# Kernel optimization log

Measured on AMD Instinct MI355X. Metric: run time of the kernel, lower is better.

## Reference

```python
import jax, jax.numpy as jnp
import numpy as np


def _gcn_conv(h, src, dst, W, b, n):
    # PyG GCNConv: XW, symmetric deg normalization (with self-loops already in src/dst), scatter-add, + bias
    hw = h @ W                                            # [n, out]
    deg = jax.ops.segment_sum(jnp.ones_like(src, dtype=h.dtype), dst, num_segments=n)
    dinv = jax.lax.rsqrt(deg)                             # deg >= 1 due to self loops
    coef = (dinv[src] * dinv[dst])[:, None]               # [E+n, 1]
    out = jax.ops.segment_sum(hw[src] * coef, dst, num_segments=n)
    return out + b


def setup_inputs() -> dict:
    key = jax.random.key(0)
    ks = jax.random.split(key, 8)
    num_users, num_items = 8192, 8192
    N = num_users + num_items
    E = 524288
    d, h1, h2, h3 = 128, 256, 128, 64
    x = jnp.arange(N, dtype=jnp.int64) if jax.config.jax_enable_x64 else jnp.arange(N, dtype=jnp.int32)
    edge_index = jax.random.randint(ks[0], (2, E), 0, N)
    emb = jax.random.normal(ks[1], (num_items + 1, d), dtype=jnp.float32)
    W1 = jax.random.normal(ks[2], (d, h1), dtype=jnp.float32) * 0.5
    b1 = jax.random.normal(ks[3], (h1,), dtype=jnp.float32) * 0.1
    W2 = jax.random.normal(ks[4], (h1, h2), dtype=jnp.float32) * 0.6
    b2 = jax.random.normal(ks[5], (h2,), dtype=jnp.float32) * 0.1
    Wl = jax.random.normal(ks[6], (h2, h3), dtype=jnp.float32) * 0.06
    bl = jax.random.normal(ks[7], (h3,), dtype=jnp.float32) * 0.1
    return {"x": x, "edge_index": edge_index, "num_users": num_users,
            "emb": emb, "W1": W1, "b1": b1, "W2": W2, "b2": b2, "Wl": Wl, "bl": bl}


def reference(x, edge_index, num_users, emb, W1, b1, W2, b2, Wl, bl):
    n = x.shape[0]
    # embedding lookup: users all use id 0, items use shifted ids
    users_e = jnp.broadcast_to(emb[0], (num_users, emb.shape[1]))
    items_e = emb[x[num_users:] - num_users + 1]
    h = jnp.concatenate([users_e, items_e], axis=0)       # [n, d]
    loops = jnp.arange(n, dtype=edge_index.dtype)
    src = jnp.concatenate([edge_index[0], loops])
    dst = jnp.concatenate([edge_index[1], loops])
    h = jax.nn.relu(_gcn_conv(h, src, dst, W1, b1, n))    # dropout p=0 -> identity
    h = jax.nn.relu(_gcn_conv(h, src, dst, W2, b2, n))
    h = jax.nn.relu(h @ Wl + bl)                          # linear + middle_function='relu'
    users = h[:num_users]
    items = h[num_users:]
    result = users @ items.T                              # [num_users, num_items]
    return jnp.clip(result, 1.0, 5.0)                     # end_function='clamp'
```

## Files before the change

### kernel.cpp

```cpp
#include <hip/hip_runtime.h>
#include <hip/hip_bf16.h>

#define CAP 96

typedef __attribute__((ext_vector_type(8))) short bf16x8;
typedef __attribute__((ext_vector_type(4))) float f32x4;

static __device__ __forceinline__ float bflo(unsigned int w) {
    union { unsigned int i; float f; } u; u.i = w << 16; return u.f;
}
static __device__ __forceinline__ float bfhi(unsigned int w) {
    union { unsigned int i; float f; } u; u.i = w & 0xffff0000u; return u.f;
}
static __device__ __forceinline__ unsigned short f2bf(float f) {
    __hip_bfloat16 h = __float2bfloat16(f);
    union { __hip_bfloat16 b; unsigned short s; } u; u.b = h; return u.s;
}

__global__ void scatter_kernel(const int* __restrict__ src, const int* __restrict__ dst,
                               int* __restrict__ wp, int* __restrict__ edges, int E) {
    int e = blockIdx.x * blockDim.x + threadIdx.x;
    if (e < E) {
        int d = dst[e];
        int p = atomicAdd(&wp[d], 1);
        if (p < CAP) edges[d * CAP + p] = src[e];
    }
}

__global__ void dinv_kernel(const int* __restrict__ wp, float* __restrict__ dinv, int n) {
    int v = blockIdx.x * blockDim.x + threadIdx.x;
    if (v < n) dinv[v] = rsqrtf((float)(wp[v] + 1));
}

__global__ void prep_kernel(const int* __restrict__ x, const float* __restrict__ emb,
                            const float* __restrict__ W1, const float* __restrict__ W2,
                            const float* __restrict__ Wl,
                            unsigned short* __restrict__ h0,
                            unsigned short* __restrict__ W1t,
                            unsigned short* __restrict__ W2t,
                            unsigned short* __restrict__ Wlt,
                            int* __restrict__ wp, int nu, int n) {
    int i = blockIdx.x * blockDim.x + threadIdx.x;
    int H = n * 16;
    if (i < H) {
        int node = i >> 4, c8 = i & 15;
        int row = (node < nu) ? 0 : (x[node] - nu + 1);
        float4 f0 = reinterpret_cast<const float4*>(emb)[(size_t)row * 32 + c8 * 2];
        float4 f1 = reinterpret_cast<const float4*>(emb)[(size_t)row * 32 + c8 * 2 + 1];
        union { unsigned short s[8]; uint4 v; } o;
        o.s[0] = f2bf(f0.x); o.s[1] = f2bf(f0.y); o.s[2] = f2bf(f0.z); o.s[3] = f2bf(f0.w);
        o.s[4] = f2bf(f1.x); o.s[5] = f2bf(f1.y); o.s[6] = f2bf(f1.z); o.s[7] = f2bf(f1.w);
        *reinterpret_cast<uint4*>(h0 + (size_t)node * 128 + c8 * 8) = o.v;
        return;
    }
    int j = i - H;
    if (j < 32768) {
        int nn = j >> 7, kk = j & 127;
        W1t[j] = f2bf(W1[kk * 256 + nn]);
        return;
    }
    if (j < 65536) {
        int jj = j - 32768;
        int nn = jj >> 8, kk = jj & 255;
        W2t[jj] = f2bf(W2[kk * 128 + nn]);
        return;
    }
    if (j < 73728) {
        int jj = j - 65536;
        int nn = jj >> 7, kk = jj & 127;
        Wlt[jj] = f2bf(Wl[kk * 64 + nn]);
        return;
    }
    int z = j - 73728;
    if (z < n) wp[z] = 0;
}

static __device__ __forceinline__ void agg_node_to_lds(
    const unsigned short* __restrict__ in, unsigned short* lds_row,
    int v, int lane, const int* __restrict__ cnt, const int* __restrict__ edges,
    const float* __restrict__ dinv, const float* __restrict__ bias, int relu) {
    int l16 = lane & 15;
    int g = lane >> 4;
    float acc[8] = {0.f, 0.f, 0.f, 0.f, 0.f, 0.f, 0.f, 0.f};
    int c = cnt[v];
    if (c > CAP) c = CAP;
    int s0 = v * CAP;
    int e = s0 + g;
    int end = s0 + c;
    for (; e + 12 < end; e += 16) {
        int sa = edges[e];
        int sb = edges[e + 4];
        int sc = edges[e + 8];
        int sd = edges[e + 12];
        float wa = dinv[sa], wb = dinv[sb], wc = dinv[sc], wd = dinv[sd];
        uint4 ra = *reinterpret_cast<const uint4*>(in + (size_t)sa * 128 + l16 * 8);
        uint4 rb = *reinterpret_cast<const uint4*>(in + (size_t)sb * 128 + l16 * 8);
        uint4 rc = *reinterpret_cast<const uint4*>(in + (size_t)sc * 128 + l16 * 8);
        uint4 rd = *reinterpret_cast<const uint4*>(in + (size_t)sd * 128 + l16 * 8);
        acc[0] = fmaf(wa, bflo(ra.x), acc[0]); acc[1] = fmaf(wa, bfhi(ra.x), acc[1]);
        acc[2] = fmaf(wa, bflo(ra.y), acc[2]); acc[3] = fmaf(wa, bfhi(ra.y), acc[3]);
        acc[4] = fmaf(wa, bflo(ra.z), acc[4]); acc[5] = fmaf(wa, bfhi(ra.z), acc[5]);
        acc[6] = fmaf(wa, bflo(ra.w), acc[6]); acc[7] = fmaf(wa, bfhi(ra.w), acc[7]);
        acc[0] = fmaf(wb, bflo(rb.x), acc[0]); acc[1] = fmaf(wb, bfhi(rb.x), acc[1]);
        acc[2] = fmaf(wb, bflo(rb.y), acc[2]); acc[3] = fmaf(wb, bfhi(rb.y), acc[3]);
        acc[4] = fmaf(wb, bflo(rb.z), acc[4]); acc[5] = fmaf(wb, bfhi(rb.z), acc[5]);
        acc[6] = fmaf(wb, bflo(rb.w), acc[6]); acc[7] = fmaf(wb, bfhi(rb.w), acc[7]);
        acc[0] = fmaf(wc, bflo(rc.x), acc[0]); acc[1] = fmaf(wc, bfhi(rc.x), acc[1]);
        acc[2] = fmaf(wc, bflo(rc.y), acc[2]); acc[3] = fmaf(wc, bfhi(rc.y), acc[3]);
        acc[4] = fmaf(wc, bflo(rc.z), acc[4]); acc[5] = fmaf(wc, bfhi(rc.z), acc[5]);
        acc[6] = fmaf(wc, bflo(rc.w), acc[6]); acc[7] = fmaf(wc, bfhi(rc.w), acc[7]);
        acc[0] = fmaf(wd, bflo(rd.x), acc[0]); acc[1] = fmaf(wd, bfhi(rd.x), acc[1]);
        acc[2] = fmaf(wd, bflo(rd.y), acc[2]); acc[3] = fmaf(wd, bfhi(rd.y), acc[3]);
        acc[4] = fmaf(wd, bflo(rd.z), acc[4]); acc[5] = fmaf(wd, bfhi(rd.z), acc[5]);
        acc[6] = fmaf(wd, bflo(rd.w), acc[6]); acc[7] = fmaf(wd, bfhi(rd.w), acc[7]);
    }
    for (; e < end; e += 4) {
        int sa = edges[e];
        float wa = dinv[sa];
        uint4 ra = *reinterpret_cast<const uint4*>(in + (size_t)sa * 128 + l16 * 8);
        acc[0] = fmaf(wa, bflo(ra.x), acc[0]); acc[1] = fmaf(wa, bfhi(ra.x), acc[1]);
        acc[2] = fmaf(wa, bflo(ra.y), acc[2]); acc[3] = fmaf(wa, bfhi(ra.y), acc[3]);
        acc[4] = fmaf(wa, bflo(ra.z), acc[4]); acc[5] = fmaf(wa, bfhi(ra.z), acc[5]);
        acc[6] = fmaf(wa, bflo(ra.w), acc[6]); acc[7] = fmaf(wa, bfhi(ra.w), acc[7]);
    }
#pragma unroll
    for (int d = 0; d < 8; ++d) {
        acc[d] += __shfl_xor(acc[d], 16, 64);
        acc[d] += __shfl_xor(acc[d], 32, 64);
    }
    if (g == 0) {
        float dv = dinv[v];
        uint4 sp = *reinterpret_cast<const uint4*>(in + (size_t)v * 128 + l16 * 8);
        float self[8] = {bflo(sp.x), bfhi(sp.x), bflo(sp.y), bfhi(sp.y),
                         bflo(sp.z), bfhi(sp.z), bflo(sp.w), bfhi(sp.w)};
        union { unsigned short s[8]; uint4 u; } o;
#pragma unroll
        for (int d = 0; d < 8; ++d) {
            float val = (acc[d] + dv * self[d]) * dv;
            if (bias) val += bias[l16 * 8 + d];
            if (relu) val = fmaxf(val, 0.f);
            o.s[d] = f2bf(val);
        }
        *reinterpret_cast<uint4*>(lds_row + l16 * 8) = o.u;
    }
}

__global__ __launch_bounds__(256) void fused_conv1_kernel(
    const unsigned short* __restrict__ h0b, unsigned short* __restrict__ hw2b,
    const int* __restrict__ cnt, const int* __restrict__ edges,
    const float* __restrict__ dinv,
    const unsigned short* __restrict__ W1t, const float* __restrict__ b1,
    const unsigned short* __restrict__ W2t) {
    __shared__ unsigned short zt[16][136];
    __shared__ unsigned short h1t[16][264];
    int wid = threadIdx.x >> 6, lane = threadIdx.x & 63;
    int base = blockIdx.x * 16;
#pragma unroll
    for (int q = 0; q < 4; ++q) {
        int loc = wid * 4 + q;
        agg_node_to_lds(h0b, &zt[loc][0], base + loc, lane, cnt, edges, dinv,
                        nullptr, 0);
    }
    __syncthreads();
    int lr = lane & 15, kg = (lane >> 4) * 8;
    int rq = (lane >> 4) * 4;
    {
        int bn = wid * 64;
        f32x4 acc[4] = {{0,0,0,0},{0,0,0,0},{0,0,0,0},{0,0,0,0}};
        for (int k0 = 0; k0 < 128; k0 += 32) {
            bf16x8 a = *reinterpret_cast<const bf16x8*>(&zt[lr][k0 + kg]);
#pragma unroll
            for (int c = 0; c < 4; ++c) {
                bf16x8 b = *reinterpret_cast<const bf16x8*>(W1t + (size_t)(bn + c * 16 + lr) * 128 + k0 + kg);
                acc[c] = __builtin_amdgcn_mfma_f32_16x16x32_bf16(a, b, acc[c], 0, 0, 0);
            }
        }
#pragma unroll
        for (int c = 0; c < 4; ++c) {
            int col = bn + c * 16 + lr;
            float bs = b1[col];
#pragma unroll
            for (int q = 0; q < 4; ++q) {
                float vv = fmaxf(acc[c][q] + bs, 0.f);
                h1t[rq + q][col] = f2bf(vv);
            }
        }
    }
    __syncthreads();
    {
        int bn = wid * 32;
        f32x4 acc[2] = {{0,0,0,0},{0,0,0,0}};
        for (int k0 = 0; k0 < 256; k0 += 32) {
            bf16x8 a = *reinterpret_cast<const bf16x8*>(&h1t[lr][k0 + kg]);
#pragma unroll
            for (int c = 0; c < 2; ++c) {
                bf16x8 b = *reinterpret_cast<const bf16x8*>(W2t + (size_t)(bn + c * 16 + lr) * 256 + k0 + kg);
                acc[c] = __builtin_amdgcn_mfma_f32_16x16x32_bf16(a, b, acc[c], 0, 0, 0);
            }
        }
#pragma unroll
        for (int c = 0; c < 2; ++c) {
            int col = bn + c * 16 + lr;
#pragma unroll
            for (int q = 0; q < 4; ++q)
                hw2b[(size_t)(base + rq + q) * 128 + col] = f2bf(acc[c][q]);
        }
    }
}

__global__ __launch_bounds__(256) void fused_conv2_kernel(
    const unsigned short* __restrict__ hw2b, unsigned short* __restrict__ h3b,
    const int* __restrict__ cnt, const int* __restrict__ edges,
    const float* __restrict__ dinv, const float* __restrict__ b2,
    const unsigned short* __restrict__ Wlt, const float* __restrict__ bl) {
    __shared__ unsigned short ht[16][136];
    int wid = threadIdx.x >> 6, lane = threadIdx.x & 63;
    int base = blockIdx.x * 16;
#pragma unroll
    for (int q = 0; q < 4; ++q) {
        int loc = wid * 4 + q;
        agg_node_to_lds(hw2b, &ht[loc][0], base + loc, lane, cnt, edges, dinv,
                        b2, 1);
    }
    __syncthreads();
    int lr = lane & 15, kg = (lane >> 4) * 8;
    int rq = (lane >> 4) * 4;
    f32x4 acc = {0, 0, 0, 0};
    for (int k0 = 0; k0 < 128; k0 += 32) {
        bf16x8 a = *reinterpret_cast<const bf16x8*>(&ht[lr][k0 + kg]);
        bf16x8 b = *reinterpret_cast<const bf16x8*>(Wlt + (size_t)(wid * 16 + lr) * 128 + k0 + kg);
        acc = __builtin_amdgcn_mfma_f32_16x16x32_bf16(a, b, acc, 0, 0, 0);
    }
    int col = wid * 16 + lr;
    float bs = bl[col];
#pragma unroll
    for (int q = 0; q < 4; ++q) {
        float vv = fmaxf(acc[q] + bs, 0.f);
        h3b[(size_t)(base + rq + q) * 64 + col] = f2bf(vv);
    }
}

__global__ __launch_bounds__(256) void final_gemm_kernel(
    const short* __restrict__ h3b, float* __restrict__ out, int nu, int ni) {
    __shared__ float tile[4][16][65];
    int wid = threadIdx.x >> 6, lane = threadIdx.x & 63;
    int row0 = blockIdx.x * 128 + (wid >> 1) * 64;
    int col0 = blockIdx.y * 128 + (wid & 1) * 64;
    int lr = lane & 15;
    int kg = (lane >> 4) * 8;
    const short* Au = h3b;
    const short* Bi = h3b + (size_t)nu * 64;
    bf16x8 a[4][2], b[4][2];
#pragma unroll
    for (int r = 0; r < 4; ++r)
#pragma unroll
        for (int kt = 0; kt < 2; ++kt) {
            a[r][kt] = *reinterpret_cast<const bf16x8*>(Au + (size_t)(row0 + r * 16 + lr) * 64 + kt * 32 + kg);
            b[r][kt] = *reinterpret_cast<const bf16x8*>(Bi + (size_t)(col0 + r * 16 + lr) * 64 + kt * 32 + kg);
        }
    f32x4 acc[4][4];
#pragma unroll
    for (int r = 0; r < 4; ++r)
#pragma unroll
        for (int c = 0; c < 4; ++c) {
            f32x4 z = {0.f, 0.f, 0.f, 0.f};
            z = __builtin_amdgcn_mfma_f32_16x16x32_bf16(a[r][0], b[c][0], z, 0, 0, 0);
            z = __builtin_amdgcn_mfma_f32_16x16x32_bf16(a[r][1], b[c][1], z, 0, 0, 0);
            acc[r][c] = z;
        }
    int rq = (lane >> 4) * 4;
    int orow = lane >> 4;
#pragma unroll
    for (int r = 0; r < 4; ++r) {
        __syncthreads();
#pragma unroll
        for (int c = 0; c < 4; ++c)
#pragma unroll
            for (int q = 0; q < 4; ++q) {
                float v = acc[r][c][q];
                v = fminf(fmaxf(v, 1.f), 5.f);
                tile[wid][rq + q][c * 16 + lr] = v;
            }
        __syncthreads();
#pragma unroll
        for (int rr = 0; rr < 4; ++rr) {
            float4 vv = *reinterpret_cast<const float4*>(&tile[wid][rr * 4 + orow][lr * 4]);
            *reinterpret_cast<float4*>(
                &out[(size_t)(row0 + r * 16 + rr * 4 + orow) * ni + col0 + lr * 4]) = vv;
        }
    }
}

extern "C" void kernel_launch(void* const* d_in, const int* in_sizes, int n_in,
                              void* d_out, int out_size, void* d_ws, size_t ws_size,
                              hipStream_t stream) {
    const int*   x   = (const int*)d_in[0];
    const int*   ei  = (const int*)d_in[1];
    const float* emb = (const float*)d_in[3];
    const float* W1  = (const float*)d_in[4];
    const float* b1  = (const float*)d_in[5];
    const float* W2  = (const float*)d_in[6];
    const float* b2  = (const float*)d_in[7];
    const float* Wl  = (const float*)d_in[8];
    const float* bl  = (const float*)d_in[9];
    float* out = (float*)d_out;

    const int n   = in_sizes[0];
    const int E   = in_sizes[1] / 2;
    const int h1d = in_sizes[5];
    const int d   = in_sizes[4] / h1d;
    const int embrows = in_sizes[3] / d;
    const int nu  = n - (embrows - 1);
    const int ni  = n - nu;

    const int* srcp = ei;
    const int* dstp = ei + E;

    char* w = (char*)d_ws;
    int*   wp      = (int*)(w + 0);
    float* dinv    = (float*)(w + (64 << 10));
    unsigned short* W1t = (unsigned short*)(w + (128 << 10));
    unsigned short* W2t = (unsigned short*)(w + (192 << 10));
    unsigned short* Wlt = (unsigned short*)(w + (256 << 10));
    int*   edges   = (int*)(w + (1 << 20));
    unsigned short* h0b  = (unsigned short*)(w + (8  << 20));
    unsigned short* hw2b = (unsigned short*)(w + (12 << 20));
    unsigned short* h3b  = (unsigned short*)(w + (16 << 20));

    {
        int total = n * 16 + 73728 + n;
        prep_kernel<<<(total + 255) / 256, 256, 0, stream>>>(
            x, emb, W1, W2, Wl, h0b, W1t, W2t, Wlt, wp, nu, n);
    }

    scatter_kernel<<<(E + 255) / 256, 256, 0, stream>>>(srcp, dstp, wp, edges, E);
    dinv_kernel<<<(n + 255) / 256, 256, 0, stream>>>(wp, dinv, n);

    fused_conv1_kernel<<<n / 16, 256, 0, stream>>>(
        h0b, hw2b, wp, edges, dinv, W1t, b1, W2t);

    fused_conv2_kernel<<<n / 16, 256, 0, stream>>>(
        hw2b, h3b, wp, edges, dinv, b2, Wlt, bl);

    {
        dim3 g(nu / 128, ni / 128);
        final_gemm_kernel<<<g, 256, 0, stream>>>((const short*)h3b, out, nu, ni);
    }
}
```

Baseline: 153.4 us.

## Split edge lists by user/item source to skip gathering identical user embeddings

Edges are bucketed per destination into separate user-source and item-source lists. In conv1 every user node shares the same embedding row, so the user-neighbour contribution collapses to a scalar sum of dinv times one row instead of a row gather per edge. This cuts roughly half the row gathers in the first aggregation and shrinks the embedding prep. The price is a second atomic counter array and per-type capacities of 64, which could truncate high-degree nodes differently than the old single cap of 96.

```diff
diff --git a/kernel.cpp b/kernel.cpp
--- a/kernel.cpp
+++ b/kernel.cpp
@@ -1,7 +1,8 @@
 #include <hip/hip_runtime.h>
 #include <hip/hip_bf16.h>
 
-#define CAP 96
+#define CAPU 64
+#define CAPI 64
 
 typedef __attribute__((ext_vector_type(8))) short bf16x8;
 typedef __attribute__((ext_vector_type(4))) float f32x4;
@@ -18,42 +19,65 @@
 }
 
 __global__ void scatter_kernel(const int* __restrict__ src, const int* __restrict__ dst,
-                               int* __restrict__ wp, int* __restrict__ edges, int E) {
+                               int* __restrict__ wpu, int* __restrict__ wpi,
+                               int* __restrict__ uedges, int* __restrict__ iedges,
+                               int nu, int E) {
     int e = blockIdx.x * blockDim.x + threadIdx.x;
     if (e < E) {
         int d = dst[e];
-        int p = atomicAdd(&wp[d], 1);
-        if (p < CAP) edges[d * CAP + p] = src[e];
-    }
-}
-
-__global__ void dinv_kernel(const int* __restrict__ wp, float* __restrict__ dinv, int n) {
+        int s = src[e];
+        if (s < nu) {
+            int p = atomicAdd(&wpu[d], 1);
+            if (p < CAPU) uedges[d * CAPU + p] = s;
+        } else {
+            int p = atomicAdd(&wpi[d], 1);
+            if (p < CAPI) iedges[d * CAPI + p] = s - nu;
+        }
+    }
+}
+
+__global__ void dinv_kernel(const int* __restrict__ wpu, const int* __restrict__ wpi,
+                            float* __restrict__ dinv, int n) {
     int v = blockIdx.x * blockDim.x + threadIdx.x;
-    if (v < n) dinv[v] = rsqrtf((float)(wp[v] + 1));
+    if (v < n) dinv[v] = rsqrtf((float)(wpu[v] + wpi[v] + 1));
 }
 
 __global__ void prep_kernel(const int* __restrict__ x, const float* __restrict__ emb,
                             const float* __restrict__ W1, const float* __restrict__ W2,
                             const float* __restrict__ Wl,
-                            unsigned short* __restrict__ h0,
+                            unsigned short* __restrict__ hi,
+                            unsigned short* __restrict__ h0u,
                             unsigned short* __restrict__ W1t,
                             unsigned short* __restrict__ W2t,
                             unsigned short* __restrict__ Wlt,
-                            int* __restrict__ wp, int nu, int n) {
+                            int* __restrict__ wpu, int* __restrict__ wpi,
+                            int nu, int n) {
     int i = blockIdx.x * blockDim.x + threadIdx.x;
-    int H = n * 16;
-    if (i < H) {
-        int node = i >> 4, c8 = i & 15;
-        int row = (node < nu) ? 0 : (x[node] - nu + 1);
+    int ni = n - nu;
+    int HI = ni * 16;
+    if (i < HI) {
+        int it = i >> 4, c8 = i & 15;
+        int row = x[nu + it] - nu + 1;
         float4 f0 = reinterpret_cast<const float4*>(emb)[(size_t)row * 32 + c8 * 2];
         float4 f1 = reinterpret_cast<const float4*>(emb)[(size_t)row * 32 + c8 * 2 + 1];
         union { unsigned short s[8]; uint4 v; } o;
         o.s[0] = f2bf(f0.x); o.s[1] = f2bf(f0.y); o.s[2] = f2bf(f0.z); o.s[3] = f2bf(f0.w);
         o.s[4] = f2bf(f1.x); o.s[5] = f2bf(f1.y); o.s[6] = f2bf(f1.z); o.s[7] = f2bf(f1.w);
-        *reinterpret_cast<uint4*>(h0 + (size_t)node * 128 + c8 * 8) = o.v;
+        *reinterpret_cast<uint4*>(hi + (size_t)it * 128 + c8 * 8) = o.v;
         return;
     }
-    int j = i - H;
+    int j = i - HI;
+    if (j < 16) {
+        int c8 = j;
+        float4 f0 = reinterpret_cast<const float4*>(emb)[c8 * 2];
+        float4 f1 = reinterpret_cast<const float4*>(emb)[c8 * 2 + 1];
+        union { unsigned short s[8]; uint4 v; } o;
+        o.s[0] = f2bf(f0.x); o.s[1] = f2bf(f0.y); o.s[2] = f2bf(f0.z); o.s[3] = f2bf(f0.w);
+        o.s[4] = f2bf(f1.x); o.s[5] = f2bf(f1.y); o.s[6] = f2bf(f1.z); o.s[7] = f2bf(f1.w);
+        *reinterpret_cast<uint4*>(h0u + c8 * 8) = o.v;
+        return;
+    }
+    j -= 16;
     if (j < 32768) {
         int nn = j >> 7, kk = j & 127;
         W1t[j] = f2bf(W1[kk * 256 + nn]);
@@ -72,31 +96,25 @@
         return;
     }
     int z = j - 73728;
-    if (z < n) wp[z] = 0;
-}
-
-static __device__ __forceinline__ void agg_node_to_lds(
-    const unsigned short* __restrict__ in, unsigned short* lds_row,
-    int v, int lane, const int* __restrict__ cnt, const int* __restrict__ edges,
-    const float* __restrict__ dinv, const float* __restrict__ bias, int relu) {
-    int l16 = lane & 15;
-    int g = lane >> 4;
-    float acc[8] = {0.f, 0.f, 0.f, 0.f, 0.f, 0.f, 0.f, 0.f};
-    int c = cnt[v];
-    if (c > CAP) c = CAP;
-    int s0 = v * CAP;
-    int e = s0 + g;
-    int end = s0 + c;
+    if (z < n) { wpu[z] = 0; return; }
+    z -= n;
+    if (z < n) { wpi[z] = 0; }
+}
+
+static __device__ __forceinline__ void gather_rows(
+    const unsigned short* __restrict__ in, int rofs,
+    const int* __restrict__ lst, int base, int cnt,
+    const float* __restrict__ dinv, int dofs,
+    int l16, int g, float acc[8]) {
+    int e = base + g, end = base + cnt;
     for (; e + 12 < end; e += 16) {
-        int sa = edges[e];
-        int sb = edges[e + 4];
-        int sc = edges[e + 8];
-        int sd = edges[e + 12];
-        float wa = dinv[sa], wb = dinv[sb], wc = dinv[sc], wd = dinv[sd];
-        uint4 ra = *reinterpret_cast<const uint4*>(in + (size_t)sa * 128 + l16 * 8);
-        uint4 rb = *reinterpret_cast<const uint4*>(in + (size_t)sb * 128 + l16 * 8);
-        uint4 rc = *reinterpret_cast<const uint4*>(in + (size_t)sc * 128 + l16 * 8);
-        uint4 rd = *reinterpret_cast<const uint4*>(in + (size_t)sd * 128 + l16 * 8);
+        int sa = lst[e], sb = lst[e + 4], sc = lst[e + 8], sd = lst[e + 12];
+        float wa = dinv[sa + dofs], wb = dinv[sb + dofs];
+        float wc = dinv[sc + dofs], wd = dinv[sd + dofs];
+        uint4 ra = *reinterpret_cast<const uint4*>(in + (size_t)(sa + rofs) * 128 + l16 * 8);
+        uint4 rb = *reinterpret_cast<const uint4*>(in + (size_t)(sb + rofs) * 128 + l16 * 8);
+        uint4 rc = *reinterpret_cast<const uint4*>(in + (size_t)(sc + rofs) * 128 + l16 * 8);
+        uint4 rd = *reinterpret_cast<const uint4*>(in + (size_t)(sd + rofs) * 128 + l16 * 8);
         acc[0] = fmaf(wa, bflo(ra.x), acc[0]); acc[1] = fmaf(wa, bfhi(ra.x), acc[1]);
         acc[2] = fmaf(wa, bflo(ra.y), acc[2]); acc[3] = fmaf(wa, bfhi(ra.y), acc[3]);
         acc[4] = fmaf(wa, bflo(ra.z), acc[4]); acc[5] = fmaf(wa, bfhi(ra.z), acc[5]);
@@ -115,51 +133,62 @@
         acc[6] = fmaf(wd, bflo(rd.w), acc[6]); acc[7] = fmaf(wd, bfhi(rd.w), acc[7]);
     }
     for (; e < end; e += 4) {
-        int sa = edges[e];
-        float wa = dinv[sa];
-        uint4 ra = *reinterpret_cast<const uint4*>(in + (size_t)sa * 128 + l16 * 8);
+        int sa = lst[e];
+        float wa = dinv[sa + dofs];
+        uint4 ra = *reinterpret_cast<const uint4*>(in + (size_t)(sa + rofs) * 128 + l16 * 8);
         acc[0] = fmaf(wa, bflo(ra.x), acc[0]); acc[1] = fmaf(wa, bfhi(ra.x), acc[1]);
         acc[2] = fmaf(wa, bflo(ra.y), acc[2]); acc[3] = fmaf(wa, bfhi(ra.y), acc[3]);
         acc[4] = fmaf(wa, bflo(ra.z), acc[4]); acc[5] = fmaf(wa, bfhi(ra.z), acc[5]);
         acc[6] = fmaf(wa, bflo(ra.w), acc[6]); acc[7] = fmaf(wa, bfhi(ra.w), acc[7]);
     }
-#pragma unroll
-    for (int d = 0; d < 8; ++d) {
-        acc[d] += __shfl_xor(acc[d], 16, 64);
-        acc[d] += __shfl_xor(acc[d], 32, 64);
-    }
-    if (g == 0) {
-        float dv = dinv[v];
-        uint4 sp = *reinterpret_cast<const uint4*>(in + (size_t)v * 128 + l16 * 8);
-        float self[8] = {bflo(sp.x), bfhi(sp.x), bflo(sp.y), bfhi(sp.y),
-                         bflo(sp.z), bfhi(sp.z), bflo(sp.w), bfhi(sp.w)};
-        union { unsigned short s[8]; uint4 u; } o;
-#pragma unroll
-        for (int d = 0; d < 8; ++d) {
-            float val = (acc[d] + dv * self[d]) * dv;
-            if (bias) val += bias[l16 * 8 + d];
-            if (relu) val = fmaxf(val, 0.f);
-            o.s[d] = f2bf(val);
-        }
-        *reinterpret_cast<uint4*>(lds_row + l16 * 8) = o.u;
-    }
 }
 
 __global__ __launch_bounds__(256) void fused_conv1_kernel(
-    const unsigned short* __restrict__ h0b, unsigned short* __restrict__ hw2b,
-    const int* __restrict__ cnt, const int* __restrict__ edges,
+    const unsigned short* __restrict__ hi, const unsigned short* __restrict__ h0u,
+    unsigned short* __restrict__ hw2b,
+    const int* __restrict__ wpu, const int* __restrict__ wpi,
+    const int* __restrict__ uedges, const int* __restrict__ iedges,
     const float* __restrict__ dinv,
     const unsigned short* __restrict__ W1t, const float* __restrict__ b1,
-    const unsigned short* __restrict__ W2t) {
+    const unsigned short* __restrict__ W2t, int nu) {
     __shared__ unsigned short zt[16][136];
     __shared__ unsigned short h1t[16][264];
     int wid = threadIdx.x >> 6, lane = threadIdx.x & 63;
+    int l16 = lane & 15, g = lane >> 4;
     int base = blockIdx.x * 16;
 #pragma unroll
     for (int q = 0; q < 4; ++q) {
-        int loc = wid * 4 + q;
-        agg_node_to_lds(h0b, &zt[loc][0], base + loc, lane, cnt, edges, dinv,
-                        nullptr, 0);
+        int v = base + wid * 4 + q;
+        float su = 0.f;
+        int cu = min(wpu[v], CAPU);
+        for (int u = lane; u < cu; u += 64) su += dinv[uedges[v * CAPU + u]];
+#pragma unroll
+        for (int off = 1; off < 64; off <<= 1) su += __shfl_xor(su, off, 64);
+        float acc[8] = {0.f, 0.f, 0.f, 0.f, 0.f, 0.f, 0.f, 0.f};
+        int ci = min(wpi[v], CAPI);
+        gather_rows(hi, 0, iedges, v * CAPI, ci, dinv, nu, l16, g, acc);
+#pragma unroll
+        for (int d = 0; d < 8; ++d) {
+            acc[d] += __shfl_xor(acc[d], 16, 64);
+            acc[d] += __shfl_xor(acc[d], 32, 64);
+        }
+        if (g == 0) {
+            float dv = dinv[v];
+            const unsigned short* selfp = (v < nu) ? h0u : (hi + (size_t)(v - nu) * 128);
+            uint4 sp = *reinterpret_cast<const uint4*>(selfp + l16 * 8);
+            uint4 hu = *reinterpret_cast<const uint4*>(h0u + l16 * 8);
+            float selff[8] = {bflo(sp.x), bfhi(sp.x), bflo(sp.y), bfhi(sp.y),
+                              bflo(sp.z), bfhi(sp.z), bflo(sp.w), bfhi(sp.w)};
+            float huf[8] = {bflo(hu.x), bfhi(hu.x), bflo(hu.y), bfhi(hu.y),
+                            bflo(hu.z), bfhi(hu.z), bflo(hu.w), bfhi(hu.w)};
+            union { unsigned short s[8]; uint4 u; } o;
+#pragma unroll
+            for (int d = 0; d < 8; ++d) {
+                float val = (acc[d] + su * huf[d] + dv * selff[d]) * dv;
+                o.s[d] = f2bf(val);
+            }
+            *reinterpret_cast<uint4*>(&zt[wid * 4 + q][l16 * 8]) = o.u;
+        }
     }
     __syncthreads();
     int lr = lane & 15, kg = (lane >> 4) * 8;
@@ -210,17 +239,41 @@
 
 __global__ __launch_bounds__(256) void fused_conv2_kernel(
     const unsigned short* __restrict__ hw2b, unsigned short* __restrict__ h3b,
-    const int* __restrict__ cnt, const int* __restrict__ edges,
+    const int* __restrict__ wpu, const int* __restrict__ wpi,
+    const int* __restrict__ uedges, const int* __restrict__ iedges,
     const float* __restrict__ dinv, const float* __restrict__ b2,
-    const unsigned short* __restrict__ Wlt, const float* __restrict__ bl) {
+    const unsigned short* __restrict__ Wlt, const float* __restrict__ bl, int nu) {
     __shared__ unsigned short ht[16][136];
     int wid = threadIdx.x >> 6, lane = threadIdx.x & 63;
+    int l16 = lane & 15, g = lane >> 4;
     int base = blockIdx.x * 16;
 #pragma unroll
     for (int q = 0; q < 4; ++q) {
-        int loc = wid * 4 + q;
-        agg_node_to_lds(hw2b, &ht[loc][0], base + loc, lane, cnt, edges, dinv,
-                        b2, 1);
+        int v = base + wid * 4 + q;
+        float acc[8] = {0.f, 0.f, 0.f, 0.f, 0.f, 0.f, 0.f, 0.f};
+        int cu = min(wpu[v], CAPU);
+        int ci = min(wpi[v], CAPI);
+        gather_rows(hw2b, 0, uedges, v * CAPU, cu, dinv, 0, l16, g, acc);
+        gather_rows(hw2b, nu, iedges, v * CAPI, ci, dinv, nu, l16, g, acc);
+#pragma unroll
+        for (int d = 0; d < 8; ++d) {
+            acc[d] += __shfl_xor(acc[d], 16, 64);
+            acc[d] += __shfl_xor(acc[d], 32, 64);
+        }
+        if (g == 0) {
+            float dv = dinv[v];
+            uint4 sp = *reinterpret_cast<const uint4*>(hw2b + (size_t)v * 128 + l16 * 8);
+            float selff[8] = {bflo(sp.x), bfhi(sp.x), bflo(sp.y), bfhi(sp.y),
+                              bflo(sp.z), bfhi(sp.z), bflo(sp.w), bfhi(sp.w)};
+            union { unsigned short s[8]; uint4 u; } o;
+#pragma unroll
+            for (int d = 0; d < 8; ++d) {
+                float val = (acc[d] + dv * selff[d]) * dv + b2[l16 * 8 + d];
+                val = fmaxf(val, 0.f);
+                o.s[d] = f2bf(val);
+            }
+            *reinterpret_cast<uint4*>(&ht[wid * 4 + q][l16 * 8]) = o.u;
+        }
     }
     __syncthreads();
     int lr = lane & 15, kg = (lane >> 4) * 8;
@@ -317,30 +370,34 @@
     const int* dstp = ei + E;
 
     char* w = (char*)d_ws;
-    int*   wp      = (int*)(w + 0);
-    float* dinv    = (float*)(w + (64 << 10));
-    unsigned short* W1t = (unsigned short*)(w + (128 << 10));
-    unsigned short* W2t = (unsigned short*)(w + (192 << 10));
-    unsigned short* Wlt = (unsigned short*)(w + (256 << 10));
-    int*   edges   = (int*)(w + (1 << 20));
-    unsigned short* h0b  = (unsigned short*)(w + (8  << 20));
+    int*   wpu     = (int*)(w + 0);
+    int*   wpi     = (int*)(w + (64 << 10));
+    float* dinv    = (float*)(w + (128 << 10));
+    unsigned short* W1t = (unsigned short*)(w + (192 << 10));
+    unsigned short* W2t = (unsigned short*)(w + (256 << 10));
+    unsigned short* Wlt = (unsigned short*)(w + (320 << 10));
+    unsigned short* h0u = (unsigned short*)(w + (340 << 10));
+    int*   uedges  = (int*)(w + (1 << 20));
+    int*   iedges  = (int*)(w + (5 << 20));
+    unsigned short* hib  = (unsigned short*)(w + (9  << 20));
     unsigned short* hw2b = (unsigned short*)(w + (12 << 20));
     unsigned short* h3b  = (unsigned short*)(w + (16 << 20));
 
     {
-        int total = n * 16 + 73728 + n;
+        int total = ni * 16 + 16 + 73728 + 2 * n;
         prep_kernel<<<(total + 255) / 256, 256, 0, stream>>>(
-            x, emb, W1, W2, Wl, h0b, W1t, W2t, Wlt, wp, nu, n);
-    }
-
-    scatter_kernel<<<(E + 255) / 256, 256, 0, stream>>>(srcp, dstp, wp, edges, E);
-    dinv_kernel<<<(n + 255) / 256, 256, 0, stream>>>(wp, dinv, n);
+            x, emb, W1, W2, Wl, hib, h0u, W1t, W2t, Wlt, wpu, wpi, nu, n);
+    }
+
+    scatter_kernel<<<(E + 255) / 256, 256, 0, stream>>>(srcp, dstp, wpu, wpi,
+                                                        uedges, iedges, nu, E);
+    dinv_kernel<<<(n + 255) / 256, 256, 0, stream>>>(wpu, wpi, dinv, n);
 
     fused_conv1_kernel<<<n / 16, 256, 0, stream>>>(
-        h0b, hw2b, wp, edges, dinv, W1t, b1, W2t);
+        hib, h0u, hw2b, wpu, wpi, uedges, iedges, dinv, W1t, b1, W2t, nu);
 
     fused_conv2_kernel<<<n / 16, 256, 0, stream>>>(
-        hw2b, h3b, wp, edges, dinv, b2, Wlt, bl);
+        hw2b, h3b, wpu, wpi, uedges, iedges, dinv, b2, Wlt, bl, nu);
 
     {
         dim3 g(nu / 128, ni / 128);
```

After: 149.4 us. 2.6% less time.
